# Optimization experiments

Measured on AMD Instinct MI355X. Metric: run time of the kernel, lower is better.

The kernel has to match this reference:

```python
import jax, jax.numpy as jnp
import numpy as np

QMAX = 127.0

def quantize_mat(mat):
    # per-row (last-dim) absmax scale, kept in fp16 like the torch code,
    # truncating cast to int8 (XLA float->int convert truncates toward zero, same as torch .to(int8))
    max_val = (jnp.max(jnp.abs(mat), axis=-1) / QMAX).astype(jnp.float16)
    q = (mat / max_val[..., None]).astype(jnp.int8)
    return q, max_val


def setup_inputs() -> dict:
    key = jax.random.key(0)
    k1, k2, k3, k4 = jax.random.split(key, 4)
    B, S, IN, OUT = 8, 4096, 2048, 2048
    x = jax.random.normal(k1, (B, S, IN), dtype=jnp.float16)
    ori_w = jax.random.normal(k2, (OUT, IN), dtype=jnp.float16)
    # SmoothQuant scales: positive, bounded away from 0 (torch clamps min=1e-5)
    scales = (jax.random.uniform(k3, (IN,), dtype=jnp.float16) + jnp.float16(0.5))
    bias = jax.random.normal(k4, (OUT,), dtype=jnp.float16)
    return {"x": x, "ori_w": ori_w, "scales": scales, "bias": bias}


def reference(x, ori_w, scales, bias):
    dtype = x.dtype
    # __init__-time: smooth the weight then quantize per output row
    w = (ori_w * scales).astype(dtype)                 # [OUT, IN]
    weight_q, w_max = quantize_mat(w)                  # int8 [OUT, IN], fp16 [OUT]
    weight_qt = weight_q.T                             # stored transposed [IN, OUT]
    # forward: smooth + quantize activations
    x = (x / scales).astype(dtype)                     # [B, S, IN]
    x_q, x_max = quantize_mat(x)                       # int8 [B,S,IN], fp16 [B,S]
    res_q = jnp.matmul(x_q.astype(jnp.float32), weight_qt.astype(jnp.float32))  # [B,S,OUT]
    # dequant factor: outer product of activation and weight scales (fp16 linear, then fp32)
    mx = (x_max[..., None] * w_max).astype(jnp.float32)  # [B,S,OUT]
    res = (res_q * mx).astype(dtype)
    res = res + bias
    return res
```

## Files before the change

kernel.cpp:

```cpp
#include <hip/hip_runtime.h>
#include <hip/hip_bf16.h>
#include <cstdint>
#include <cstddef>

#define M_TOT 32768
#define N_OUT 2048
#define K_IN  2048

typedef int   v4i __attribute__((ext_vector_type(4)));
typedef float v4f __attribute__((ext_vector_type(4)));

__device__ __forceinline__ void gload16(const int8_t* g, int8_t* l) {
  __builtin_amdgcn_global_load_lds(
      (const __attribute__((address_space(1))) void*)g,
      (__attribute__((address_space(3))) void*)l, 16, 0, 0);
}

__global__ __launch_bounds__(256) void quant_rows_wave(
    const float* __restrict__ in,
    const float* __restrict__ scales,
    int8_t* __restrict__ q, float* __restrict__ rmax,
    int nrows, int mul_mode)
{
  const int wib = threadIdx.x >> 6, lane = threadIdx.x & 63;
  for (int row = blockIdx.x * 4 + wib; row < nrows; row += gridDim.x * 4) {
    const float* rp = in + (size_t)row * K_IN;
    _Float16 xs[32];
    float amax = 0.f;
#pragma unroll
    for (int c = 0; c < 8; ++c) {
      const int off = c * 256 + lane * 4;
      const v4f xv = __builtin_nontemporal_load((const v4f*)(rp + off));
      const v4f sv = *(const v4f*)(scales + off);
#pragma unroll
      for (int j = 0; j < 4; ++j) {
        const _Float16 hx = (_Float16)xv[j];
        const _Float16 hs = (_Float16)sv[j];
        const _Float16 v = mul_mode ? (_Float16)(hx * hs) : (_Float16)(hx / hs);
        xs[c * 4 + j] = v;
        amax = fmaxf(amax, fabsf((float)v));
      }
    }
#pragma unroll
    for (int off = 32; off; off >>= 1) amax = fmaxf(amax, __shfl_xor(amax, off));
    _Float16 hqm = (_Float16)amax / (_Float16)127.0f;
    if (lane == 0) rmax[row] = (float)hqm;
    if (hqm == (_Float16)0.f) hqm = (_Float16)1.0f;
#pragma unroll
    for (int c = 0; c < 8; ++c) {
      int8_t qb[4];
#pragma unroll
      for (int j = 0; j < 4; ++j) {
        const float qf = (float)(_Float16)(xs[c * 4 + j] / hqm);
        qb[j] = (int8_t)(int)qf;
      }
      int pk;
      __builtin_memcpy(&pk, qb, 4);
      *(int*)(q + (size_t)row * K_IN + c * 256 + lane * 4) = pk;
    }
  }
}

__global__ __launch_bounds__(512, 2) void gemm_i8_kernel(
    const int8_t* __restrict__ Aq, const int8_t* __restrict__ Bq,
    const float* __restrict__ Am, const float* __restrict__ Bm,
    const float* __restrict__ bias, float* __restrict__ out)
{
  __shared__ __align__(16) int8_t lds[8 * 16384];
  const int tid = threadIdx.x;
  const int w = tid >> 6, lane = tid & 63;
  const int wm = w >> 2, wn = w & 3;
  const int bx = blockIdx.x & 7;
  const int by = blockIdx.x >> 3;
  const long bm = (long)by * 256;
  const int  bn = bx * 256;

  const int schunk = ((lane & 3) ^ ((lane >> 3) & 3)) * 16;
  const int srow = w * 16 + (lane >> 2);
  const int8_t* gA = Aq + (bm + srow) * (long)K_IN + schunk;
  const int8_t* gB = Bq + ((long)(bn + srow)) * K_IN + schunk;

  const int fr = lane & 15, fq = lane >> 4;
  const int pc = (fq ^ ((fr >> 1) & 3)) * 16;
  const int aoff = (wm * 128 + fr) * 64 + pc;
  const int boff = (wn * 64  + fr) * 64 + pc;

  v4i acc[8][4] = {};
  v4i afr[4], bfr[4];

#define STAGE(G) do {                                                         \
    const int g_ = (G);                                                       \
    const long koff_ = (long)((g_ >> 2) * 128 + ((g_ >> 1) & 1) * 64);        \
    int8_t* const ld_ = lds + (g_ & 7) * 16384 + w * 1024;                    \
    const int8_t* const gp_ = (g_ & 1) ? gB : gA;                             \
    gload16(gp_ + koff_,                  ld_);                               \
    gload16(gp_ + koff_ + 128L * K_IN,    ld_ + 8192);                        \
  } while (0)

#define VMCNT(N) asm volatile("s_waitcnt vmcnt(" #N ")" ::: "memory")
#define BAR() do { asm volatile("" ::: "memory");                             \
                   __builtin_amdgcn_s_barrier();                              \
                   asm volatile("" ::: "memory"); } while (0)

#define READS(T, KH, MH) do {                                                 \
    const int sa_ = (((T) & 1) * 4 + (KH) * 2) * 16384;                       \
    if ((MH) == 0) {                                                          \
      _Pragma("unroll")                                                       \
      for (int ni = 0; ni < 4; ++ni)                                          \
        bfr[ni] = *(const v4i*)(lds + sa_ + 16384 + boff + ni * 1024);        \
    }                                                                         \
    _Pragma("unroll")                                                         \
    for (int mi = 0; mi < 4; ++mi)                                            \
      afr[mi] = *(const v4i*)(lds + sa_ + aoff + ((MH) * 64 + mi * 16) * 64); \
  } while (0)

#define MFMA16(MH) do {                                                       \
    __builtin_amdgcn_s_setprio(1);                                            \
    _Pragma("unroll")                                                         \
    for (int mi = 0; mi < 4; ++mi)                                            \
      _Pragma("unroll")                                                       \
      for (int ni = 0; ni < 4; ++ni)                                          \
        acc[(MH) * 4 + mi][ni] = __builtin_amdgcn_mfma_i32_16x16x64_i8(       \
            afr[mi], bfr[ni], acc[(MH) * 4 + mi][ni], 0, 0, 0);               \
    __builtin_amdgcn_s_setprio(0);                                            \
  } while (0)

  STAGE(0); STAGE(1); STAGE(2); STAGE(3); STAGE(4); STAGE(5);
  VMCNT(8); BAR();

#pragma unroll 2
  for (int t = 0; t < 14; ++t) {
    READS(t, 0, 0); STAGE(4 * t + 6); VMCNT(8); BAR(); MFMA16(0); BAR();
    READS(t, 0, 1); STAGE(4 * t + 7); VMCNT(8); BAR(); MFMA16(1); BAR();
    READS(t, 1, 0); STAGE(4 * t + 8); VMCNT(8); BAR(); MFMA16(0); BAR();
    READS(t, 1, 1); STAGE(4 * t + 9); VMCNT(8); BAR(); MFMA16(1); BAR();
  }
  READS(14, 0, 0); STAGE(62); VMCNT(8); BAR(); MFMA16(0); BAR();
  READS(14, 0, 1); STAGE(63); VMCNT(8); BAR(); MFMA16(1); BAR();
  READS(14, 1, 0);             BAR(); MFMA16(0); BAR();
  READS(14, 1, 1); VMCNT(4);   BAR(); MFMA16(1); BAR();
  READS(15, 0, 0);                              BAR(); MFMA16(0); BAR();
  READS(15, 0, 1); VMCNT(0);   BAR(); MFMA16(1); BAR();
  READS(15, 1, 0); MFMA16(0);
  READS(15, 1, 1); MFMA16(1);

#undef STAGE
#undef VMCNT
#undef BAR
#undef READS
#undef MFMA16

  const long cm0 = bm + wm * 128;
  const int  cn0 = bn + wn * 64;
  float amv[8][4];
#pragma unroll
  for (int mi = 0; mi < 8; ++mi)
#pragma unroll
    for (int r = 0; r < 4; ++r)
      amv[mi][r] = Am[cm0 + mi * 16 + fq * 4 + r];
#pragma unroll
  for (int ni = 0; ni < 4; ++ni) {
    const int col = cn0 + ni * 16 + fr;
    const float wmv = Bm[col];
    const _Float16 bsv = (_Float16)bias[col];
#pragma unroll
    for (int mi = 0; mi < 8; ++mi) {
#pragma unroll
      for (int r = 0; r < 4; ++r) {
        const long row = cm0 + mi * 16 + fq * 4 + r;
        const float mx = (float)(_Float16)((_Float16)amv[mi][r] * (_Float16)wmv);
        const _Float16 resh = (_Float16)((float)acc[mi][ni][r] * mx);
        __builtin_nontemporal_store((float)(_Float16)(resh + bsv),
                                    out + row * N_OUT + col);
      }
    }
  }
}

extern "C" void kernel_launch(void* const* d_in, const int* in_sizes, int n_in,
                              void* d_out, int out_size, void* d_ws, size_t ws_size,
                              hipStream_t stream) {
  const float* x      = (const float*)d_in[0];
  const float* ori_w  = (const float*)d_in[1];
  const float* scales = (const float*)d_in[2];
  const float* bias   = (const float*)d_in[3];
  float* out = (float*)d_out;

  int8_t* xq = (int8_t*)d_ws;
  int8_t* wq = xq + (size_t)M_TOT * K_IN;
  float*  xm = (float*)(wq + (size_t)N_OUT * K_IN);
  float*  wmx = xm + M_TOT;

  quant_rows_wave<<<2048, 256, 0, stream>>>(x, scales, xq, xm, M_TOT, 0);
  quant_rows_wave<<<512,  256, 0, stream>>>(ori_w, scales, wq, wmx, N_OUT, 1);

  gemm_i8_kernel<<<dim3(1024), 512, 0, stream>>>(xq, wq, xm, wmx, bias, out);
}
```

Baseline: 587.8 us.

## Merge half-tile MFMA phases into full regions with one barrier each

New measurement: 583.1 us. Within noise of the previous version (-0.8%).

```diff
diff --git a/kernel.cpp b/kernel.cpp
--- a/kernel.cpp
+++ b/kernel.cpp
@@ -86,7 +86,6 @@
   const int boff = (wn * 64  + fr) * 64 + pc;
 
   v4i acc[8][4] = {};
-  v4i afr[4], bfr[4];
 
 #define STAGE(G) do {                                                         \
     const int g_ = (G);                                                       \
@@ -102,53 +101,41 @@
                    __builtin_amdgcn_s_barrier();                              \
                    asm volatile("" ::: "memory"); } while (0)
 
-#define READS(T, KH, MH) do {                                                 \
+#define REGION(T, KH) do {                                                    \
     const int sa_ = (((T) & 1) * 4 + (KH) * 2) * 16384;                       \
-    if ((MH) == 0) {                                                          \
+    v4i afr[8], bfr[4];                                                       \
+    _Pragma("unroll")                                                         \
+    for (int ni = 0; ni < 4; ++ni)                                            \
+      bfr[ni] = *(const v4i*)(lds + sa_ + 16384 + boff + ni * 1024);          \
+    _Pragma("unroll")                                                         \
+    for (int mi = 0; mi < 8; ++mi)                                            \
+      afr[mi] = *(const v4i*)(lds + sa_ + aoff + mi * 1024);                  \
+    __builtin_amdgcn_s_setprio(1);                                            \
+    _Pragma("unroll")                                                         \
+    for (int mi = 0; mi < 8; ++mi)                                            \
       _Pragma("unroll")                                                       \
       for (int ni = 0; ni < 4; ++ni)                                          \
-        bfr[ni] = *(const v4i*)(lds + sa_ + 16384 + boff + ni * 1024);        \
-    }                                                                         \
-    _Pragma("unroll")                                                         \
-    for (int mi = 0; mi < 4; ++mi)                                            \
-      afr[mi] = *(const v4i*)(lds + sa_ + aoff + ((MH) * 64 + mi * 16) * 64); \
-  } while (0)
-
-#define MFMA16(MH) do {                                                       \
-    __builtin_amdgcn_s_setprio(1);                                            \
-    _Pragma("unroll")                                                         \
-    for (int mi = 0; mi < 4; ++mi)                                            \
-      _Pragma("unroll")                                                       \
-      for (int ni = 0; ni < 4; ++ni)                                          \
-        acc[(MH) * 4 + mi][ni] = __builtin_amdgcn_mfma_i32_16x16x64_i8(       \
-            afr[mi], bfr[ni], acc[(MH) * 4 + mi][ni], 0, 0, 0);               \
+        acc[mi][ni] = __builtin_amdgcn_mfma_i32_16x16x64_i8(                  \
+            afr[mi], bfr[ni], acc[mi][ni], 0, 0, 0);                          \
     __builtin_amdgcn_s_setprio(0);                                            \
   } while (0)
 
-  STAGE(0); STAGE(1); STAGE(2); STAGE(3); STAGE(4); STAGE(5);
-  VMCNT(8); BAR();
+  STAGE(0); STAGE(1); STAGE(2); STAGE(3);
 
 #pragma unroll 2
   for (int t = 0; t < 14; ++t) {
-    READS(t, 0, 0); STAGE(4 * t + 6); VMCNT(8); BAR(); MFMA16(0); BAR();
-    READS(t, 0, 1); STAGE(4 * t + 7); VMCNT(8); BAR(); MFMA16(1); BAR();
-    READS(t, 1, 0); STAGE(4 * t + 8); VMCNT(8); BAR(); MFMA16(0); BAR();
-    READS(t, 1, 1); STAGE(4 * t + 9); VMCNT(8); BAR(); MFMA16(1); BAR();
+    STAGE(4 * t + 4); STAGE(4 * t + 5); VMCNT(4); BAR(); REGION(t, 0);
+    STAGE(4 * t + 6); STAGE(4 * t + 7); VMCNT(4); BAR(); REGION(t, 1);
   }
-  READS(14, 0, 0); STAGE(62); VMCNT(8); BAR(); MFMA16(0); BAR();
-  READS(14, 0, 1); STAGE(63); VMCNT(8); BAR(); MFMA16(1); BAR();
-  READS(14, 1, 0);             BAR(); MFMA16(0); BAR();
-  READS(14, 1, 1); VMCNT(4);   BAR(); MFMA16(1); BAR();
-  READS(15, 0, 0);                              BAR(); MFMA16(0); BAR();
-  READS(15, 0, 1); VMCNT(0);   BAR(); MFMA16(1); BAR();
-  READS(15, 1, 0); MFMA16(0);
-  READS(15, 1, 1); MFMA16(1);
+  STAGE(60); STAGE(61); VMCNT(4); BAR(); REGION(14, 0);
+  STAGE(62); STAGE(63); VMCNT(4); BAR(); REGION(14, 1);
+  VMCNT(4); BAR(); REGION(15, 0);
+  VMCNT(0); BAR(); REGION(15, 1);
 
 #undef STAGE
 #undef VMCNT
 #undef BAR
-#undef READS
-#undef MFMA16
+#undef REGION
 
   const long cm0 = bm + wm * 128;
   const int  cn0 = bn + wn * 64;
```
